# Kernel tuning notes

Measured on AMD Instinct MI355X. Metric: run time of the kernel, lower is better.

Reference implementation:

```python
import jax, jax.numpy as jnp
import numpy as np
from jax import lax

B, H, W, C, PS = 2, 192, 192, 96, 8
NWH, NWW = H // PS, W // PS
NW = NWH * NWW  # 576 windows
P2 = PS * PS    # 64


def dwconv3x3(x, w):
    # x: [B, C, H, W], w: [C, 1, 3, 3] depthwise
    return lax.conv_general_dilated(x, w, (1, 1), 'SAME',
                                    dimension_numbers=('NCHW', 'OIHW', 'NCHW'),
                                    feature_group_count=x.shape[1])


def conv1x1(x, w):
    # x: [B, Cin, H, W], w: [Cout, Cin]
    return jnp.einsum('bchw,oc->bohw', x, w)


def patchify(t):
    # t: [B, C, H, W] -> [B*C, nW, ps^2]  (window partition, per-channel tokens)
    t = t.reshape(B, C, NWH, PS, NWW, PS).transpose(0, 1, 2, 4, 3, 5)
    return t.reshape(B * C, NW, P2)


def unpatchify(t):
    # [B*C, nW, ps^2] -> [B, C, H, W]  (window reverse)
    t = t.reshape(B, C, NWH, NWW, PS, PS).transpose(0, 1, 2, 4, 3, 5)
    return t.reshape(B, C, H, W)


def l2norm(t):
    # F.normalize(dim=-1), eps=1e-12
    n = jnp.sqrt(jnp.sum(t * t, axis=-1, keepdims=True))
    return t / jnp.maximum(n, 1e-12)


def setup_inputs() -> dict:
    key = jax.random.key(0)
    ks = jax.random.split(key, 8)
    s = 0.05
    return {
        'x': jax.random.normal(ks[0], (B, H * W, C), jnp.float32),
        'qkv_w': jax.random.normal(ks[1], (3 * C, C), jnp.float32) * s,
        'qkv_dw_w': jax.random.normal(ks[2], (3 * C, 1, 3, 3), jnp.float32) * s,
        'scale': jnp.ones((1, 1, 1), jnp.float32),  # num_heads = 1
        'proj_w': jax.random.normal(ks[3], (C, C), jnp.float32) * s,
        'proj_b': jax.random.normal(ks[4], (C,), jnp.float32) * s,
        'pe_w1': jax.random.normal(ks[5], (C, 1, 3, 3), jnp.float32) * s,
        'pe_w2': jax.random.normal(ks[6], (C, 1, 3, 3), jnp.float32) * s,
    }


def reference(x, qkv_w, qkv_dw_w, scale, proj_w, proj_b, pe_w1, pe_w2):
    xi = x.transpose(0, 2, 1).reshape(B, C, H, W)
    qkv = dwconv3x3(conv1x1(xi, qkv_w), qkv_dw_w)      # [B, 3C, H, W]
    q, k, v_in = jnp.split(qkv, 3, axis=1)             # each [B, C, H, W]

    qp = l2norm(patchify(q))                           # [B*C, nW, ps^2]
    kp = l2norm(patchify(k))
    vp = patchify(v_in)

    logits = jnp.einsum('bnp,bmp->bnm', qp, kp) * scale  # [B*C, nW, nW]
    attn = jax.nn.softmax(logits, axis=-1)
    o = jnp.einsum('bnm,bmp->bnp', attn, vp)             # [B*C, nW, ps^2]

    xo = unpatchify(o)                                   # [B, C, H, W]
    out_c = conv1x1(xo, proj_w) + proj_b[None, :, None, None]
    pe = dwconv3x3(jax.nn.gelu(dwconv3x3(v_in, pe_w1), approximate=False), pe_w2)
    out = out_c + pe                                     # [B, C, H, W]
    return out.reshape(B, C, H * W).transpose(0, 2, 1)   # [B, L, C]
```

## Files before the change

kernel.cpp:

```cpp
#include <hip/hip_runtime.h>
#include <hip/hip_bf16.h>
#include <math.h>

#define BB   2
#define CC   96
#define C3   288
#define HH   192
#define WWI  192
#define HWQ  (HH*WWI)
#define NWH  24
#define NW   576
#define P2   64

typedef float v4f  __attribute__((ext_vector_type(4)));
typedef float f32x4 __attribute__((ext_vector_type(4)));
typedef short s16x8 __attribute__((ext_vector_type(8)));
typedef short s16x4 __attribute__((ext_vector_type(4)));
typedef unsigned short ushort_t;

static __device__ __forceinline__ unsigned short f2bf(float f) {
  __hip_bfloat16 h = __float2bfloat16(f);
  return *reinterpret_cast<unsigned short*>(&h);
}
static __device__ __forceinline__ float bf2f(ushort_t u) {
  union { unsigned u32; float f; } x;
  x.u32 = ((unsigned)u) << 16;
  return x.f;
}

__global__ __launch_bounds__(256) void k0_cvtw(const float* __restrict__ w,
                                               ushort_t* __restrict__ wb, int n) {
  int i = blockIdx.x * 256 + threadIdx.x;
  if (i < n) wb[i] = f2bf(w[i]);
}

__global__ __launch_bounds__(384) void k1_qkv(const float* __restrict__ x,
                                              const ushort_t* __restrict__ qwb,
                                              ushort_t* __restrict__ qkv_bf) {
  const int tid  = threadIdx.x;
  const int lane = tid & 63;
  const int wv   = tid >> 6;
  const int lq   = lane & 15;
  const int g    = lane >> 4;
  const int m0   = blockIdx.x * 64;
  const int b    = m0 / HWQ;
  const int hwb  = m0 % HWQ;
  const int n0   = wv * 48;

  const f32x4 zf = {0.f, 0.f, 0.f, 0.f};
  f32x4 acc[4][3];
#pragma unroll
  for (int mt = 0; mt < 4; mt++)
#pragma unroll
    for (int nt = 0; nt < 3; nt++) acc[mt][nt] = zf;

#pragma unroll
  for (int kk = 0; kk < 3; kk++) {
    s16x8 af[4];
#pragma unroll
    for (int mt = 0; mt < 4; mt++) {
      const float* xr = x + (size_t)(m0 + mt * 16 + lq) * 96 + kk * 32 + g * 8;
      v4f x0 = *(const v4f*)xr;
      v4f x1 = *(const v4f*)(xr + 4);
      s16x8 a;
#pragma unroll
      for (int t = 0; t < 4; t++) {
        a[t]     = (short)f2bf(x0[t]);
        a[4 + t] = (short)f2bf(x1[t]);
      }
      af[mt] = a;
    }
    s16x8 bfr[3];
#pragma unroll
    for (int nt = 0; nt < 3; nt++)
      bfr[nt] = *(const s16x8*)(qwb + (size_t)(n0 + nt * 16 + lq) * 96 + kk * 32 + g * 8);
#pragma unroll
    for (int mt = 0; mt < 4; mt++)
#pragma unroll
      for (int nt = 0; nt < 3; nt++)
        acc[mt][nt] = __builtin_amdgcn_mfma_f32_16x16x32_bf16(af[mt], bfr[nt], acc[mt][nt], 0, 0, 0);
  }

  ushort_t* ob = qkv_bf + (size_t)b * C3 * HWQ;
#pragma unroll
  for (int nt = 0; nt < 3; nt++) {
    int o = n0 + nt * 16 + lq;
#pragma unroll
    for (int mt = 0; mt < 4; mt++) {
      s16x4 st;
#pragma unroll
      for (int t = 0; t < 4; t++) st[t] = (short)f2bf(acc[mt][nt][t]);
      *(s16x4*)(ob + (size_t)o * HWQ + hwb + mt * 16 + g * 4) = st;
    }
  }
}

__global__ __launch_bounds__(256) void k2_dw(const ushort_t* __restrict__ qkv_pre,
                                             const float* __restrict__ dww,
                                             ushort_t* __restrict__ qpo, ushort_t* __restrict__ kpo,
                                             ushort_t* __restrict__ vpo) {
  __shared__ float tin[34][40];
  int bx  = blockIdx.x;
  int b   = bx / (C3 * 36);
  int rem = bx % (C3 * 36);
  int ch  = rem / 36;
  int tile = rem % 36;
  int ty = tile / 6, tx = tile % 6;
  int tid = threadIdx.x;
  const ushort_t* src = qkv_pre + ((size_t)b * C3 + ch) * HWQ;
  const int h0 = ty * 32 - 1, w0 = tx * 32;

  for (int idx = tid; idx < 340; idx += 256) {
    int r = idx / 10, u = idx - r * 10;
    int h = h0 + r;
    bool hok = (h >= 0 && h < HH);
    if (u < 8) {
      v4f f = {0.f, 0.f, 0.f, 0.f};
      if (hok) {
        s16x4 raw = *(const s16x4*)(src + h * WWI + w0 + u * 4);
#pragma unroll
        for (int t = 0; t < 4; t++) f[t] = bf2f((ushort_t)raw[t]);
      }
      *(v4f*)&tin[r][4 + u * 4] = f;
    } else {
      int w = (u == 8) ? (w0 - 1) : (w0 + 32);
      int cdst = (u == 8) ? 3 : 36;
      float f = 0.f;
      if (hok && w >= 0 && w < WWI) f = bf2f(src[h * WWI + w]);
      tin[r][cdst] = f;
    }
  }
  float wv[9];
#pragma unroll
  for (int i = 0; i < 9; i++) wv[i] = dww[ch * 9 + i];
  __syncthreads();

  const int part = ch / CC, c96 = ch % CC;
  const int bc = b * CC + c96;
  const int cc = tid & 31;
  const int s  = tid >> 5;
  const int r0 = 4 * s;

  float a0 = tin[r0][cc + 3],     a1 = tin[r0][cc + 4],     a2 = tin[r0][cc + 5];
  float b0 = tin[r0 + 1][cc + 3], b1 = tin[r0 + 1][cc + 4], b2 = tin[r0 + 1][cc + 5];
  float o[4];
  float ssq = 0.f;
#pragma unroll
  for (int i = 0; i < 4; i++) {
    float c0 = tin[r0 + 2 + i][cc + 3];
    float c1 = tin[r0 + 2 + i][cc + 4];
    float c2 = tin[r0 + 2 + i][cc + 5];
    float acc = wv[0] * a0 + wv[1] * a1 + wv[2] * a2
              + wv[3] * b0 + wv[4] * b1 + wv[5] * b2
              + wv[6] * c0 + wv[7] * c1 + wv[8] * c2;
    o[i] = acc;
    ssq += acc * acc;
    a0 = b0; a1 = b1; a2 = b2;
    b0 = c0; b1 = c1; b2 = c2;
  }

  float inv = 1.f;
  if (part != 2) {
    float t = ssq;
    t += __shfl_xor(t, 1, 64);
    t += __shfl_xor(t, 2, 64);
    t += __shfl_xor(t, 4, 64);
    t += __shfl_xor(t, 32, 64);
    inv = 1.f / fmaxf(sqrtf(t), 1e-12f);
  }

  ushort_t* dst = (part == 0) ? qpo : ((part == 1) ? kpo : vpo);
  int n = (ty * 4 + (s >> 1)) * NWH + tx * 4 + (cc >> 3);
  int prow0 = r0 & 7;
  int pcol  = cc & 7;
  ushort_t* op = dst + ((size_t)bc * NW + n) * P2;
#pragma unroll
  for (int i = 0; i < 4; i++)
    op[(prow0 + i) * 8 + pcol] = f2bf(o[i] * inv);
}

__device__ __forceinline__ void stage_v(const ushort_t* __restrict__ vb,
                                        ushort_t* __restrict__ dst, int tid) {
#pragma unroll
  for (int it = 0; it < 3; it++) {
    int idx = tid + it * 192;
    if (it < 2 || idx < 512) {
      int kv = idx & 63, c = idx >> 6;
      s16x8 v = *(const s16x8*)(vb + kv * 64 + c * 8);
#pragma unroll
      for (int t = 0; t < 8; t++) {
        int p = c * 8 + t;
        dst[p * 64 + (kv ^ ((p & 7) << 3))] = (ushort_t)v[t];
      }
    }
  }
}

__device__ __forceinline__ void stage_k(const ushort_t* __restrict__ kb,
                                        ushort_t* __restrict__ dst, int tid) {
#pragma unroll
  for (int it = 0; it < 3; it++) {
    int idx = tid + it * 192;
    if (it < 2 || idx < 512) {
      int kv = idx >> 3, c = idx & 7;
      s16x8 v = *(const s16x8*)(kb + kv * 64 + c * 8);
      *(s16x8*)&dst[kv * 64 + ((c * 8) ^ ((kv & 7) << 3))] = v;
    }
  }
}

__global__ __launch_bounds__(192, 2) void k3_attn(const ushort_t* __restrict__ qp,
                                                  const ushort_t* __restrict__ kp,
                                                  const ushort_t* __restrict__ vp,
                                                  const float* __restrict__ scale_p,
                                                  float* __restrict__ o_p) {
  __shared__ ushort_t VT[2][4096];
  __shared__ ushort_t KT[2][4096];
  const int tid  = threadIdx.x;
  const int lane = tid & 63;
  const int wv   = tid >> 6;
  const int lq   = lane & 15;
  const int g    = lane >> 4;
  const int bid  = blockIdx.x;
  const int gw   = (bid & 7) * 144 + (bid >> 3);
  const int bc   = gw / 6;
  const int qch  = gw % 6;
  const int q0   = qch * 96 + wv * 32;
  const float sl = scale_p[0];

  const ushort_t* qpb = qp + (size_t)bc * NW * 64;
  const ushort_t* kpb = kp + (size_t)bc * NW * 64;
  const ushort_t* vpb = vp + (size_t)bc * NW * 64;

  s16x8 qf[2][2];
#pragma unroll
  for (int nt = 0; nt < 2; nt++)
#pragma unroll
    for (int ks = 0; ks < 2; ks++)
      qf[nt][ks] = *(const s16x8*)(qpb + (size_t)(q0 + nt * 16 + lq) * 64 + ks * 32 + g * 8);

  const f32x4 zf = {0.f, 0.f, 0.f, 0.f};
  f32x4 Oa[2][4];
#pragma unroll
  for (int a = 0; a < 2; a++)
#pragma unroll
    for (int b2 = 0; b2 < 4; b2++) Oa[a][b2] = zf;
  float lsum[2] = {0.f, 0.f};

  stage_k(kpb, KT[0], tid);
  stage_v(vpb, VT[0], tid);
  __syncthreads();

  const int s0 = lq + ((lane & 16) << 1);

  for (int kt = 0; kt < 9; kt++) {
    const int cur = kt & 1;
    if (kt < 8) {
      stage_k(kpb + (kt + 1) * 4096, KT[cur ^ 1], tid);
      stage_v(vpb + (kt + 1) * 4096, VT[cur ^ 1], tid);
    }

    f32x4 s[4][2];
#pragma unroll
    for (int a = 0; a < 4; a++)
#pragma unroll
      for (int b2 = 0; b2 < 2; b2++) s[a][b2] = zf;
#pragma unroll
    for (int ks = 0; ks < 2; ks++) {
      s16x8 kf[4];
#pragma unroll
      for (int mt = 0; mt < 4; mt++)
        kf[mt] = *(const s16x8*)&KT[cur][(mt * 16 + lq) * 64 + ((ks * 32 + g * 8) ^ ((lq & 7) << 3))];
#pragma unroll
      for (int mt = 0; mt < 4; mt++)
#pragma unroll
        for (int nt = 0; nt < 2; nt++)
          s[mt][nt] = __builtin_amdgcn_mfma_f32_16x16x32_bf16(kf[mt], qf[nt][ks], s[mt][nt], 0, 0, 0);
    }

    unsigned pk[2][4][2];
#pragma unroll
    for (int nt = 0; nt < 2; nt++) {
      float rs = 0.f;
#pragma unroll
      for (int mt = 0; mt < 4; mt++) {
        float e0 = __expf(s[mt][nt][0] * sl);
        float e1 = __expf(s[mt][nt][1] * sl);
        float e2 = __expf(s[mt][nt][2] * sl);
        float e3 = __expf(s[mt][nt][3] * sl);
        rs += (e0 + e1) + (e2 + e3);
        pk[nt][mt][0] = (unsigned)f2bf(e0) | ((unsigned)f2bf(e1) << 16);
        pk[nt][mt][1] = (unsigned)f2bf(e2) | ((unsigned)f2bf(e3) << 16);
      }
      lsum[nt] += rs;
    }

#pragma unroll
    for (int ks2 = 0; ks2 < 2; ks2++) {
      s16x8 vf[4];
#pragma unroll
      for (int ntd = 0; ntd < 4; ntd++) {
        int p = ntd * 16 + lq;
        vf[ntd] = *(const s16x8*)&VT[cur][p * 64 + ((ks2 * 32 + g * 8) ^ ((p & 7) << 3))];
      }
#pragma unroll
      for (int qt = 0; qt < 2; qt++) {
        union { s16x8 v; unsigned u[4]; } af;
#pragma unroll
        for (int w = 0; w < 4; w++) {
          int src = s0 + ((w >> 1) << 4);
          unsigned lo = __shfl(pk[qt][2 * ks2 + 0][w & 1], src, 64);
          unsigned hi = __shfl(pk[qt][2 * ks2 + 1][w & 1], src, 64);
          af.u[w] = (lane & 32) ? hi : lo;
        }
#pragma unroll
        for (int ntd = 0; ntd < 4; ntd++)
          Oa[qt][ntd] = __builtin_amdgcn_mfma_f32_16x16x32_bf16(af.v, vf[ntd], Oa[qt][ntd], 0, 0, 0);
      }
    }
    __syncthreads();
  }

  float inv[2];
#pragma unroll
  for (int nt = 0; nt < 2; nt++) {
    float v = lsum[nt];
    v += __shfl_xor(v, 16, 64);
    v += __shfl_xor(v, 32, 64);
    inv[nt] = 1.f / v;
  }
  float* ob = o_p + ((size_t)bc * NW + q0) * 64;
#pragma unroll
  for (int qt = 0; qt < 2; qt++) {
#pragma unroll
    for (int r = 0; r < 4; r++) {
      float iv = __shfl(inv[qt], g * 4 + r, 64);
#pragma unroll
      for (int ntd = 0; ntd < 4; ntd++)
        ob[(qt * 16 + g * 4 + r) * 64 + ntd * 16 + lq] = Oa[qt][ntd][r] * iv;
    }
  }
}

__global__ __launch_bounds__(256) void k4_pe(const ushort_t* __restrict__ vp,
                                             const float* __restrict__ w1p,
                                             const float* __restrict__ w2p,
                                             float* __restrict__ pe) {
  __shared__ float vt[36][38];
  __shared__ float gt[34][36];
  int bx = blockIdx.x;
  int b = bx / (CC * 36);
  int rem = bx % (CC * 36);
  int c = rem / 36;
  int tile = rem % 36;
  int ty = tile / 6, tx = tile % 6;
  int tid = threadIdx.x;
  const ushort_t* src = vp + ((size_t)(b * CC + c)) * NW * P2;
  int h0 = ty * 32 - 2, w0 = tx * 32 - 2;
  for (int idx = tid; idx < 36 * 36; idx += 256) {
    int r = idx / 36, cc2 = idx % 36;
    int h = h0 + r, w = w0 + cc2;
    float v = 0.f;
    if (h >= 0 && h < HH && w >= 0 && w < WWI) {
      int n2 = (h >> 3) * NWH + (w >> 3);
      int p2 = ((h & 7) << 3) | (w & 7);
      v = bf2f(src[(size_t)n2 * P2 + p2]);
    }
    vt[r][cc2] = v;
  }
  __syncthreads();
  float w1[9], w2[9];
#pragma unroll
  for (int i = 0; i < 9; i++) { w1[i] = w1p[c * 9 + i]; w2[i] = w2p[c * 9 + i]; }
  for (int idx = tid; idx < 34 * 34; idx += 256) {
    int r = idx / 34, cc2 = idx % 34;
    int gh = ty * 32 + r - 1, gw = tx * 32 + cc2 - 1;
    float a = 0.f;
#pragma unroll
    for (int dy = 0; dy < 3; dy++)
#pragma unroll
      for (int dx = 0; dx < 3; dx++)
        a += w1[dy * 3 + dx] * vt[r + dy][cc2 + dx];
    float gv = 0.5f * a * (1.f + erff(a * 0.70710678118f));
    gt[r][cc2] = (gh >= 0 && gh < HH && gw >= 0 && gw < WWI) ? gv : 0.f;
  }
  __syncthreads();
  float* dst = pe + ((size_t)(b * CC + c)) * HWQ;
  for (int idx = tid; idx < 1024; idx += 256) {
    int hl = idx >> 5, wl = idx & 31;
    float a = 0.f;
#pragma unroll
    for (int dy = 0; dy < 3; dy++)
#pragma unroll
      for (int dx = 0; dx < 3; dx++)
        a += w2[dy * 3 + dx] * gt[hl + dy][wl + dx];
    dst[(ty * 32 + hl) * WWI + tx * 32 + wl] = a;
  }
}

__global__ __launch_bounds__(384) void k5_proj(const float* __restrict__ o_p,
                                               const ushort_t* __restrict__ pwb,
                                               const float* __restrict__ pb,
                                               const float* __restrict__ pe,
                                               float* __restrict__ out) {
  __shared__ float xo[96][68];
  const int bx = blockIdx.x;
  const int b = bx / NW, n = bx % NW;
  const int wr = n / NWH, wc = n % NWH;
  const int tid = threadIdx.x;
  for (int idx = tid; idx < 96 * 16; idx += 384) {
    int c = idx >> 4, p4 = idx & 15;
    *(v4f*)&xo[c][p4 * 4] =
        *(const v4f*)(o_p + ((size_t)(b * CC + c) * NW + n) * P2 + p4 * 4);
  }
  __syncthreads();
  const int lane = tid & 63, wv = tid >> 6;
  const int lq = lane & 15, g = lane >> 4;
  const int o = wv * 16 + lq;
  s16x8 bfr[3];
#pragma unroll
  for (int kk = 0; kk < 3; kk++)
    bfr[kk] = *(const s16x8*)(pwb + (size_t)o * 96 + kk * 32 + g * 8);
  const f32x4 zf = {0.f, 0.f, 0.f, 0.f};
  f32x4 acc[4] = {zf, zf, zf, zf};
#pragma unroll
  for (int kk = 0; kk < 3; kk++) {
#pragma unroll
    for (int mt = 0; mt < 4; mt++) {
      s16x8 a;
#pragma unroll
      for (int j = 0; j < 8; j++)
        a[j] = (short)f2bf(xo[kk * 32 + g * 8 + j][mt * 16 + lq]);
      acc[mt] = __builtin_amdgcn_mfma_f32_16x16x32_bf16(a, bfr[kk], acc[mt], 0, 0, 0);
    }
  }
  const float pbv = pb[o];
  const float* per = pe + ((size_t)(b * CC + o)) * HWQ;
  float* ob = out + (size_t)b * HWQ * CC;
#pragma unroll
  for (int mt = 0; mt < 4; mt++) {
    int p = mt * 16 + g * 4;
    int hw = (wr * 8 + (p >> 3)) * WWI + wc * 8 + (p & 7);
    v4f pv = *(const v4f*)(per + hw);
#pragma unroll
    for (int r = 0; r < 4; r++)
      ob[(size_t)(hw + r) * CC + o] = acc[mt][r] + pbv + pv[r];
  }
}

extern "C" void kernel_launch(void* const* d_in, const int* in_sizes, int n_in,
                              void* d_out, int out_size, void* d_ws, size_t ws_size,
                              hipStream_t stream) {
  const float* x        = (const float*)d_in[0];
  const float* qkv_w    = (const float*)d_in[1];
  const float* qkv_dw_w = (const float*)d_in[2];
  const float* scale    = (const float*)d_in[3];
  const float* proj_w   = (const float*)d_in[4];
  const float* proj_b   = (const float*)d_in[5];
  const float* pe_w1    = (const float*)d_in[6];
  const float* pe_w2    = (const float*)d_in[7];
  float* ws = (float*)d_ws;

  ushort_t* qkv_bf = (ushort_t*)ws;
  float*    o_p    = ws;
  float*    pe     = ws + 10616832;
  ushort_t* qp     = (ushort_t*)(ws + 17694720);
  ushort_t* kp     = (ushort_t*)(ws + 21233664);
  ushort_t* vp     = (ushort_t*)(ws + 24772608);
  ushort_t* qwb    = (ushort_t*)(ws + 28311552);
  ushort_t* pwb    = (ushort_t*)(ws + 28325376);

  float* out = (float*)d_out;

  hipLaunchKernelGGL(k0_cvtw, dim3(108), dim3(256), 0, stream, qkv_w, qwb, C3 * CC);
  hipLaunchKernelGGL(k0_cvtw, dim3(36), dim3(256), 0, stream, proj_w, pwb, CC * CC);
  hipLaunchKernelGGL(k1_qkv, dim3((BB * HWQ) / 64), dim3(384), 0, stream, x, qwb, qkv_bf);
  hipLaunchKernelGGL(k2_dw, dim3(BB * C3 * 36), dim3(256), 0, stream,
                     qkv_bf, qkv_dw_w, qp, kp, vp);
  hipLaunchKernelGGL(k3_attn, dim3(BB * CC * 6), dim3(192), 0, stream, qp, kp, vp, scale, o_p);
  hipLaunchKernelGGL(k4_pe, dim3(BB * CC * 36), dim3(256), 0, stream, vp, pe_w1, pe_w2, pe);
  hipLaunchKernelGGL(k5_proj, dim3(BB * NW), dim3(384), 0, stream, o_p, pwb, proj_b, pe, out);
}
```

Measured before the change: 176.3 us.

## Pre-swizzle K and transpose V in global memory during depthwise conv stage

The depthwise-conv kernel now writes K and V straight into the per-tile swizzled (and, for V, transposed) layout that the attention kernel keeps in shared memory. The attention kernel's staging then becomes a plain contiguous 16-byte copy, with no per-element scattered LDS stores for V. The cost moves to k2's global stores, which become more scattered for V, and to the PE kernel, which must read V through the swizzled indexing.

Result: slower. 193.9 us (+10.0%).

```diff
diff --git a/kernel.cpp b/kernel.cpp
--- a/kernel.cpp
+++ b/kernel.cpp
@@ -97,8 +97,8 @@
 
 __global__ __launch_bounds__(256) void k2_dw(const ushort_t* __restrict__ qkv_pre,
                                              const float* __restrict__ dww,
-                                             ushort_t* __restrict__ qpo, ushort_t* __restrict__ kpo,
-                                             ushort_t* __restrict__ vpo) {
+                                             ushort_t* __restrict__ qpo, ushort_t* __restrict__ kpt,
+                                             ushort_t* __restrict__ vpt) {
   __shared__ float tin[34][40];
   int bx  = blockIdx.x;
   int b   = bx / (C3 * 36);
@@ -169,49 +169,45 @@
     inv = 1.f / fmaxf(sqrtf(t), 1e-12f);
   }
 
-  ushort_t* dst = (part == 0) ? qpo : ((part == 1) ? kpo : vpo);
-  int n = (ty * 4 + (s >> 1)) * NWH + tx * 4 + (cc >> 3);
-  int prow0 = r0 & 7;
-  int pcol  = cc & 7;
-  ushort_t* op = dst + ((size_t)bc * NW + n) * P2;
-#pragma unroll
-  for (int i = 0; i < 4; i++)
-    op[(prow0 + i) * 8 + pcol] = f2bf(o[i] * inv);
-}
-
-__device__ __forceinline__ void stage_v(const ushort_t* __restrict__ vb,
-                                        ushort_t* __restrict__ dst, int tid) {
+  const int n = (ty * 4 + (s >> 1)) * NWH + tx * 4 + (cc >> 3);
+  const int prow0 = r0 & 7;
+  const int pcol  = cc & 7;
+  const int ntile = n >> 6, kvl = n & 63;
+  if (part == 0) {
+    ushort_t* op = qpo + ((size_t)bc * NW + n) * P2;
+#pragma unroll
+    for (int i = 0; i < 4; i++)
+      op[(prow0 + i) * 8 + pcol] = f2bf(o[i] * inv);
+  } else if (part == 1) {
+    ushort_t* op = kpt + ((size_t)(bc * 9 + ntile) * 64 + kvl) * 64;
+    const int sw = (kvl & 7) << 3;
+#pragma unroll
+    for (int i = 0; i < 4; i++)
+      op[((prow0 + i) * 8 + pcol) ^ sw] = f2bf(o[i] * inv);
+  } else {
+    ushort_t* opb = vpt + (size_t)(bc * 9 + ntile) * 4096;
+    const int swv = pcol << 3;
+#pragma unroll
+    for (int i = 0; i < 4; i++) {
+      int p = (prow0 + i) * 8 + pcol;
+      opb[p * 64 + (kvl ^ swv)] = f2bf(o[i]);
+    }
+  }
+}
+
+__device__ __forceinline__ void stage_cp(const ushort_t* __restrict__ srcT,
+                                         ushort_t* __restrict__ dst, int tid) {
 #pragma unroll
   for (int it = 0; it < 3; it++) {
     int idx = tid + it * 192;
-    if (it < 2 || idx < 512) {
-      int kv = idx & 63, c = idx >> 6;
-      s16x8 v = *(const s16x8*)(vb + kv * 64 + c * 8);
-#pragma unroll
-      for (int t = 0; t < 8; t++) {
-        int p = c * 8 + t;
-        dst[p * 64 + (kv ^ ((p & 7) << 3))] = (ushort_t)v[t];
-      }
-    }
-  }
-}
-
-__device__ __forceinline__ void stage_k(const ushort_t* __restrict__ kb,
-                                        ushort_t* __restrict__ dst, int tid) {
-#pragma unroll
-  for (int it = 0; it < 3; it++) {
-    int idx = tid + it * 192;
-    if (it < 2 || idx < 512) {
-      int kv = idx >> 3, c = idx & 7;
-      s16x8 v = *(const s16x8*)(kb + kv * 64 + c * 8);
-      *(s16x8*)&dst[kv * 64 + ((c * 8) ^ ((kv & 7) << 3))] = v;
-    }
+    if (it < 2 || idx < 512)
+      *(s16x8*)&dst[idx * 8] = *(const s16x8*)(srcT + idx * 8);
   }
 }
 
 __global__ __launch_bounds__(192, 2) void k3_attn(const ushort_t* __restrict__ qp,
-                                                  const ushort_t* __restrict__ kp,
-                                                  const ushort_t* __restrict__ vp,
+                                                  const ushort_t* __restrict__ kpt,
+                                                  const ushort_t* __restrict__ vpt,
                                                   const float* __restrict__ scale_p,
                                                   float* __restrict__ o_p) {
   __shared__ ushort_t VT[2][4096];
@@ -228,9 +224,9 @@
   const int q0   = qch * 96 + wv * 32;
   const float sl = scale_p[0];
 
-  const ushort_t* qpb = qp + (size_t)bc * NW * 64;
-  const ushort_t* kpb = kp + (size_t)bc * NW * 64;
-  const ushort_t* vpb = vp + (size_t)bc * NW * 64;
+  const ushort_t* qpb  = qp  + (size_t)bc * NW * 64;
+  const ushort_t* kptb = kpt + (size_t)bc * 9 * 4096;
+  const ushort_t* vptb = vpt + (size_t)bc * 9 * 4096;
 
   s16x8 qf[2][2];
 #pragma unroll
@@ -247,8 +243,8 @@
     for (int b2 = 0; b2 < 4; b2++) Oa[a][b2] = zf;
   float lsum[2] = {0.f, 0.f};
 
-  stage_k(kpb, KT[0], tid);
-  stage_v(vpb, VT[0], tid);
+  stage_cp(kptb, KT[0], tid);
+  stage_cp(vptb, VT[0], tid);
   __syncthreads();
 
   const int s0 = lq + ((lane & 16) << 1);
@@ -256,8 +252,8 @@
   for (int kt = 0; kt < 9; kt++) {
     const int cur = kt & 1;
     if (kt < 8) {
-      stage_k(kpb + (kt + 1) * 4096, KT[cur ^ 1], tid);
-      stage_v(vpb + (kt + 1) * 4096, VT[cur ^ 1], tid);
+      stage_cp(kptb + (kt + 1) * 4096, KT[cur ^ 1], tid);
+      stage_cp(vptb + (kt + 1) * 4096, VT[cur ^ 1], tid);
     }
 
     f32x4 s[4][2];
@@ -342,7 +338,7 @@
   }
 }
 
-__global__ __launch_bounds__(256) void k4_pe(const ushort_t* __restrict__ vp,
+__global__ __launch_bounds__(256) void k4_pe(const ushort_t* __restrict__ vpt,
                                              const float* __restrict__ w1p,
                                              const float* __restrict__ w2p,
                                              float* __restrict__ pe) {
@@ -355,7 +351,7 @@
   int tile = rem % 36;
   int ty = tile / 6, tx = tile % 6;
   int tid = threadIdx.x;
-  const ushort_t* src = vp + ((size_t)(b * CC + c)) * NW * P2;
+  const ushort_t* src = vpt + (size_t)(b * CC + c) * 9 * 4096;
   int h0 = ty * 32 - 2, w0 = tx * 32 - 2;
   for (int idx = tid; idx < 36 * 36; idx += 256) {
     int r = idx / 36, cc2 = idx % 36;
@@ -364,7 +360,7 @@
     if (h >= 0 && h < HH && w >= 0 && w < WWI) {
       int n2 = (h >> 3) * NWH + (w >> 3);
       int p2 = ((h & 7) << 3) | (w & 7);
-      v = bf2f(src[(size_t)n2 * P2 + p2]);
+      v = bf2f(src[((size_t)(n2 >> 6) * 64 + p2) * 64 + ((n2 & 63) ^ ((p2 & 7) << 3))]);
     }
     vt[r][cc2] = v;
   }
@@ -465,8 +461,8 @@
   float*    o_p    = ws;
   float*    pe     = ws + 10616832;
   ushort_t* qp     = (ushort_t*)(ws + 17694720);
-  ushort_t* kp     = (ushort_t*)(ws + 21233664);
-  ushort_t* vp     = (ushort_t*)(ws + 24772608);
+  ushort_t* kpt    = (ushort_t*)(ws + 21233664);
+  ushort_t* vpt    = (ushort_t*)(ws + 24772608);
   ushort_t* qwb    = (ushort_t*)(ws + 28311552);
   ushort_t* pwb    = (ushort_t*)(ws + 28325376);
 
@@ -476,8 +472,8 @@
   hipLaunchKernelGGL(k0_cvtw, dim3(36), dim3(256), 0, stream, proj_w, pwb, CC * CC);
   hipLaunchKernelGGL(k1_qkv, dim3((BB * HWQ) / 64), dim3(384), 0, stream, x, qwb, qkv_bf);
   hipLaunchKernelGGL(k2_dw, dim3(BB * C3 * 36), dim3(256), 0, stream,
-                     qkv_bf, qkv_dw_w, qp, kp, vp);
-  hipLaunchKernelGGL(k3_attn, dim3(BB * CC * 6), dim3(192), 0, stream, qp, kp, vp, scale, o_p);
-  hipLaunchKernelGGL(k4_pe, dim3(BB * CC * 36), dim3(256), 0, stream, vp, pe_w1, pe_w2, pe);
+                     qkv_bf, qkv_dw_w, qp, kpt, vpt);
+  hipLaunchKernelGGL(k3_attn, dim3(BB * CC * 6), dim3(192), 0, stream, qp, kpt, vpt, scale, o_p);
+  hipLaunchKernelGGL(k4_pe, dim3(BB * CC * 36), dim3(256), 0, stream, vpt, pe_w1, pe_w2, pe);
   hipLaunchKernelGGL(k5_proj, dim3(BB * NW), dim3(384), 0, stream, o_p, pwb, proj_b, pe, out);
 }
```

## Halve per-wave query rows in attention and add MFMA priority hints

Applied to the files above, without the earlier changes.

The attention kernel now gives each wave 16 query windows instead of 32, doubling the grid to 2304 blocks of 48 queries each. It also wraps the two MFMA phases in s_setprio raises so matrix work is favoured over other waves. The aim is more blocks for better CU occupancy and load balance and lower register pressure. The cost is that every K/V tile is staged from global memory twice as often, since each block now covers half as many queries.

Measured after the change: 185.0 us. 1.05x slower.

```diff
diff --git a/kernel.cpp b/kernel.cpp
--- a/kernel.cpp
+++ b/kernel.cpp
@@ -222,30 +222,26 @@
   const int lq   = lane & 15;
   const int g    = lane >> 4;
   const int bid  = blockIdx.x;
-  const int gw   = (bid & 7) * 144 + (bid >> 3);
-  const int bc   = gw / 6;
-  const int qch  = gw % 6;
-  const int q0   = qch * 96 + wv * 32;
+  const int gw   = (bid & 7) * 288 + (bid >> 3);
+  const int bc   = gw / 12;
+  const int qch  = gw % 12;
+  const int q0   = qch * 48 + wv * 16;
   const float sl = scale_p[0];
 
   const ushort_t* qpb = qp + (size_t)bc * NW * 64;
   const ushort_t* kpb = kp + (size_t)bc * NW * 64;
   const ushort_t* vpb = vp + (size_t)bc * NW * 64;
 
-  s16x8 qf[2][2];
-#pragma unroll
-  for (int nt = 0; nt < 2; nt++)
-#pragma unroll
-    for (int ks = 0; ks < 2; ks++)
-      qf[nt][ks] = *(const s16x8*)(qpb + (size_t)(q0 + nt * 16 + lq) * 64 + ks * 32 + g * 8);
+  s16x8 qf[2];
+#pragma unroll
+  for (int ks = 0; ks < 2; ks++)
+    qf[ks] = *(const s16x8*)(qpb + (size_t)(q0 + lq) * 64 + ks * 32 + g * 8);
 
   const f32x4 zf = {0.f, 0.f, 0.f, 0.f};
-  f32x4 Oa[2][4];
-#pragma unroll
-  for (int a = 0; a < 2; a++)
-#pragma unroll
-    for (int b2 = 0; b2 < 4; b2++) Oa[a][b2] = zf;
-  float lsum[2] = {0.f, 0.f};
+  f32x4 Oa[4];
+#pragma unroll
+  for (int b2 = 0; b2 < 4; b2++) Oa[b2] = zf;
+  float lsum = 0.f;
 
   stage_k(kpb, KT[0], tid);
   stage_v(vpb, VT[0], tid);
@@ -260,11 +256,10 @@
       stage_v(vpb + (kt + 1) * 4096, VT[cur ^ 1], tid);
     }
 
-    f32x4 s[4][2];
-#pragma unroll
-    for (int a = 0; a < 4; a++)
-#pragma unroll
-      for (int b2 = 0; b2 < 2; b2++) s[a][b2] = zf;
+    f32x4 s[4];
+#pragma unroll
+    for (int a = 0; a < 4; a++) s[a] = zf;
+    __builtin_amdgcn_s_setprio(1);
 #pragma unroll
     for (int ks = 0; ks < 2; ks++) {
       s16x8 kf[4];
@@ -273,28 +268,27 @@
         kf[mt] = *(const s16x8*)&KT[cur][(mt * 16 + lq) * 64 + ((ks * 32 + g * 8) ^ ((lq & 7) << 3))];
 #pragma unroll
       for (int mt = 0; mt < 4; mt++)
-#pragma unroll
-        for (int nt = 0; nt < 2; nt++)
-          s[mt][nt] = __builtin_amdgcn_mfma_f32_16x16x32_bf16(kf[mt], qf[nt][ks], s[mt][nt], 0, 0, 0);
-    }
-
-    unsigned pk[2][4][2];
-#pragma unroll
-    for (int nt = 0; nt < 2; nt++) {
+        s[mt] = __builtin_amdgcn_mfma_f32_16x16x32_bf16(kf[mt], qf[ks], s[mt], 0, 0, 0);
+    }
+    __builtin_amdgcn_s_setprio(0);
+
+    unsigned pk[4][2];
+    {
       float rs = 0.f;
 #pragma unroll
       for (int mt = 0; mt < 4; mt++) {
-        float e0 = __expf(s[mt][nt][0] * sl);
-        float e1 = __expf(s[mt][nt][1] * sl);
-        float e2 = __expf(s[mt][nt][2] * sl);
-        float e3 = __expf(s[mt][nt][3] * sl);
+        float e0 = __expf(s[mt][0] * sl);
+        float e1 = __expf(s[mt][1] * sl);
+        float e2 = __expf(s[mt][2] * sl);
+        float e3 = __expf(s[mt][3] * sl);
         rs += (e0 + e1) + (e2 + e3);
-        pk[nt][mt][0] = (unsigned)f2bf(e0) | ((unsigned)f2bf(e1) << 16);
-        pk[nt][mt][1] = (unsigned)f2bf(e2) | ((unsigned)f2bf(e3) << 16);
-      }
-      lsum[nt] += rs;
-    }
-
+        pk[mt][0] = (unsigned)f2bf(e0) | ((unsigned)f2bf(e1) << 16);
+        pk[mt][1] = (unsigned)f2bf(e2) | ((unsigned)f2bf(e3) << 16);
+      }
+      lsum += rs;
+    }
+
+    __builtin_amdgcn_s_setprio(1);
 #pragma unroll
     for (int ks2 = 0; ks2 < 2; ks2++) {
       s16x8 vf[4];
@@ -303,42 +297,33 @@
         int p = ntd * 16 + lq;
         vf[ntd] = *(const s16x8*)&VT[cur][p * 64 + ((ks2 * 32 + g * 8) ^ ((p & 7) << 3))];
       }
-#pragma unroll
-      for (int qt = 0; qt < 2; qt++) {
-        union { s16x8 v; unsigned u[4]; } af;
-#pragma unroll
-        for (int w = 0; w < 4; w++) {
-          int src = s0 + ((w >> 1) << 4);
-          unsigned lo = __shfl(pk[qt][2 * ks2 + 0][w & 1], src, 64);
-          unsigned hi = __shfl(pk[qt][2 * ks2 + 1][w & 1], src, 64);
-          af.u[w] = (lane & 32) ? hi : lo;
-        }
-#pragma unroll
-        for (int ntd = 0; ntd < 4; ntd++)
-          Oa[qt][ntd] = __builtin_amdgcn_mfma_f32_16x16x32_bf16(af.v, vf[ntd], Oa[qt][ntd], 0, 0, 0);
-      }
-    }
+      union { s16x8 v; unsigned u[4]; } af;
+#pragma unroll
+      for (int w = 0; w < 4; w++) {
+        int src = s0 + ((w >> 1) << 4);
+        unsigned lo = __shfl(pk[2 * ks2 + 0][w & 1], src, 64);
+        unsigned hi = __shfl(pk[2 * ks2 + 1][w & 1], src, 64);
+        af.u[w] = (lane & 32) ? hi : lo;
+      }
+#pragma unroll
+      for (int ntd = 0; ntd < 4; ntd++)
+        Oa[ntd] = __builtin_amdgcn_mfma_f32_16x16x32_bf16(af.v, vf[ntd], Oa[ntd], 0, 0, 0);
+    }
+    __builtin_amdgcn_s_setprio(0);
     __syncthreads();
   }
 
-  float inv[2];
-#pragma unroll
-  for (int nt = 0; nt < 2; nt++) {
-    float v = lsum[nt];
-    v += __shfl_xor(v, 16, 64);
-    v += __shfl_xor(v, 32, 64);
-    inv[nt] = 1.f / v;
-  }
+  float v = lsum;
+  v += __shfl_xor(v, 16, 64);
+  v += __shfl_xor(v, 32, 64);
+  const float inv = 1.f / v;
   float* ob = o_p + ((size_t)bc * NW + q0) * 64;
 #pragma unroll
-  for (int qt = 0; qt < 2; qt++) {
-#pragma unroll
-    for (int r = 0; r < 4; r++) {
-      float iv = __shfl(inv[qt], g * 4 + r, 64);
-#pragma unroll
-      for (int ntd = 0; ntd < 4; ntd++)
-        ob[(qt * 16 + g * 4 + r) * 64 + ntd * 16 + lq] = Oa[qt][ntd][r] * iv;
-    }
+  for (int r = 0; r < 4; r++) {
+    float iv = __shfl(inv, g * 4 + r, 64);
+#pragma unroll
+    for (int ntd = 0; ntd < 4; ntd++)
+      ob[(g * 4 + r) * 64 + ntd * 16 + lq] = Oa[ntd][r] * iv;
   }
 }
 
@@ -477,7 +462,7 @@
   hipLaunchKernelGGL(k1_qkv, dim3((BB * HWQ) / 64), dim3(384), 0, stream, x, qwb, qkv_bf);
   hipLaunchKernelGGL(k2_dw, dim3(BB * C3 * 36), dim3(256), 0, stream,
                      qkv_bf, qkv_dw_w, qp, kp, vp);
-  hipLaunchKernelGGL(k3_attn, dim3(BB * CC * 6), dim3(192), 0, stream, qp, kp, vp, scale, o_p);
+  hipLaunchKernelGGL(k3_attn, dim3(BB * CC * 12), dim3(192), 0, stream, qp, kp, vp, scale, o_p);
   hipLaunchKernelGGL(k4_pe, dim3(BB * CC * 36), dim3(256), 0, stream, vp, pe_w1, pe_w2, pe);
   hipLaunchKernelGGL(k5_proj, dim3(BB * NW), dim3(384), 0, stream, o_p, pwb, proj_b, pe, out);
 }
```
